# Performance work log

Hardware: AMD Instinct MI355X
Metric: run time of the kernel (lower is better)

The kernel has to match this reference:

```python
import jax, jax.numpy as jnp
import numpy as np

REF_MIC_IDX = 0
LOAD = 0.001 / np.sqrt(2.0)  # diagonal loading added to BOTH real and imag parts in the torch code


def setup_inputs() -> dict:
    key = jax.random.key(0)
    k1, k2, k3 = jax.random.split(key, 3)
    shape = (8, 2, 8, 600, 257)  # N, RI, C, T, F
    return {
        "mixture": jax.random.normal(k1, shape, dtype=jnp.float32),
        "target": jax.random.normal(k2, shape, dtype=jnp.float32),
        "noise": jax.random.normal(k3, shape, dtype=jnp.float32),
    }


def _to_complex(x):
    # (N, 2, C, T, F) RI-stacked -> (N, C, T, F) complex
    return jax.lax.complex(x[:, 0], x[:, 1])


def reference(mixture, target, noise):
    N, _, C, T, F = mixture.shape
    y = _to_complex(mixture)  # (N, C, T, F)
    v = _to_complex(noise)
    cdtype = y.dtype

    # Time-averaged spatial covariance: sum_t V V^H / T -> (N, F, C, C)
    # (fused; the original materializes per-frame C x C matrices then sums)
    phi_v = jnp.einsum("nctf,ndtf->nfcd", v, jnp.conj(v)) / T
    phi_y = jnp.einsum("nctf,ndtf->nfcd", y, jnp.conj(y)) / T

    eye = jnp.eye(C, dtype=cdtype)
    # torch adds LOAD*eye to both real and imag slices -> complex (1+1j)*LOAD*eye
    phi_v = phi_v + (LOAD * (1.0 + 1.0j)) * eye

    G = jnp.linalg.inv(phi_v) @ phi_y  # (N, F, C, C)

    # l = trace(G) - C, where torch subtracts scalar C from both RI parts
    l = jnp.trace(G, axis1=-2, axis2=-1) - (C * (1.0 + 1.0j))  # (N, F)

    # H = (1/l) * (G - I) e_ref  -> column ref_mic_idx of (G - I)
    Ge = (G - eye)[..., :, REF_MIC_IDX]  # (N, F, C)
    H = Ge / l[..., None]  # (N, F, C)

    # Beamform: X(n,t,f) = sum_c conj(H)_{n,f,c} * y_{n,c,t,f}
    X = jnp.einsum("nfc,nctf->ntf", jnp.conj(H), y)  # (N, T, F)

    # Output in RI-stacked form with singleton channel: (N, 2, 1, T, F)
    est = jnp.stack([jnp.real(X), jnp.imag(X)], axis=1)[:, :, None]
    return est
```

## Files before the change

### kernel.cpp

```cpp
#include <hip/hip_runtime.h>
#include <stdint.h>


constexpr int N_  = 8;
constexpr int C_  = 8;
constexpr int T_  = 600;
constexpr int F_  = 257;
constexpr int TF_  = T_ * F_;
constexpr int CTF_ = C_ * TF_;
constexpr int NSTR_ = 2 * CTF_;
constexpr int NF_  = N_ * F_;
constexpr int NPAIR_ = 36;
constexpr float LOADC_ = 7.0710678118654755e-4f;
constexpr float INV_T_ = 1.0f / 600.0f;

struct cx { float r, i; };
__device__ __forceinline__ cx cmul(cx a, cx b) { return {a.r*b.r - a.i*b.i, a.r*b.i + a.i*b.r}; }
__device__ __forceinline__ cx csub(cx a, cx b) { return {a.r - b.r, a.i - b.i}; }
__device__ __forceinline__ cx cconj(cx a) { return {a.r, -a.i}; }
__device__ __forceinline__ cx cinv(cx a) {
    float id = 1.0f / (a.r*a.r + a.i*a.i);
    return {a.r*id, -a.i*id};
}
__device__ __forceinline__ cx cmadd(cx acc, cx a, cx b) {
    acc.r += a.r*b.r - a.i*b.i;
    acc.i += a.r*b.i + a.i*b.r;
    return acc;
}

__device__ __forceinline__ void gload_lds4(const float* g, float* l) {
    __builtin_amdgcn_global_load_lds(
        (const __attribute__((address_space(1))) void*)g,
        (__attribute__((address_space(3))) void*)l,
        4, 0, 0);
}

#define VMWAIT(N) asm volatile("s_waitcnt vmcnt(" #N ")" ::: "memory")
#define LGKM0()   asm volatile("s_waitcnt lgkmcnt(0)" ::: "memory")

template<int TSPLIT>
__global__ __launch_bounds__(64, 1) void cov_partial(
        const float* __restrict__ mix, const float* __restrict__ noi,
        float* __restrict__ part) {
    constexpr int TCHUNK = T_ / TSPLIT;
    constexpr int P = 3;
    static_assert(TCHUNK % P == 0 && TCHUNK > P, "ring/chunk mismatch");

    __shared__ float S[P][16][64];

    const int lane = threadIdx.x;
    const int f = blockIdx.x * 64 + lane;
    if (f >= F_) return;
    const int n = blockIdx.y;
    const int z = blockIdx.z;
    const int m = z & 1;
    const int chunk = z >> 1;
    const float* src = (m ? mix : noi) + (size_t)n * NSTR_
                     + (size_t)(chunk * TCHUNK) * F_ + f;

    auto stage = [&](int s, int t) {
        const float* pg = src + (size_t)t * F_;
        float* lp = &S[s][0][0];
#pragma unroll
        for (int c = 0; c < C_; ++c) {
            gload_lds4(pg + (size_t)c * TF_,        lp + (2*c)   * 64);
            gload_lds4(pg + (size_t)c * TF_ + CTF_, lp + (2*c+1) * 64);
        }
    };

    float accr[NPAIR_], acci[NPAIR_];
#pragma unroll
    for (int p = 0; p < NPAIR_; ++p) { accr[p] = 0.f; acci[p] = 0.f; }

    auto consume = [&](int s) {
        float re[C_], im[C_];
#pragma unroll
        for (int c = 0; c < C_; ++c) {
            re[c] = S[s][2*c][lane];
            im[c] = S[s][2*c+1][lane];
        }
        int p = 0;
#pragma unroll
        for (int c = 0; c < C_; ++c) {
#pragma unroll
            for (int d = 0; d <= c; ++d, ++p) {
                accr[p] += re[c]*re[d] + im[c]*im[d];
                acci[p] += im[c]*re[d] - re[c]*im[d];
            }
        }
    };

    stage(0, 0); stage(1, 1); stage(2, 2);

    for (int tb = 0; tb < TCHUNK - P; tb += P) {
        VMWAIT(32); consume(0); LGKM0(); stage(0, tb + 3);
        VMWAIT(32); consume(1); LGKM0(); stage(1, tb + 4);
        VMWAIT(32); consume(2); LGKM0(); stage(2, tb + 5);
    }
    VMWAIT(32); consume(0);
    VMWAIT(16); consume(1);
    VMWAIT(0);  consume(2);

    float* out = part + (size_t)((m * TSPLIT + chunk) * 72) * NF_ + n * F_ + f;
#pragma unroll
    for (int p = 0; p < NPAIR_; ++p) {
        out[(size_t)(2*p)   * NF_] = accr[p];
        out[(size_t)(2*p+1) * NF_] = acci[p];
    }
}

__global__ __launch_bounds__(256) void reduce_cov(float* __restrict__ part, int tsplit) {
    int flat = blockIdx.x * 256 + threadIdx.x;
    constexpr int NQ4 = NF_ / 4;
    if (flat >= 2 * 72 * NQ4) return;
    int idx4 = flat % NQ4;
    int z = flat / NQ4;
    int m = z / 72;
    int q = z % 72;
    const float4* p4 = (const float4*)(part) + ((size_t)((m * tsplit) * 72 + q) * NF_) / 4 + idx4;
    float4 s = {0.f, 0.f, 0.f, 0.f};
    for (int ch = 0; ch < tsplit; ++ch) {
        float4 v = p4[(size_t)(ch * 72) * NF_ / 4];
        s.x += v.x; s.y += v.y; s.z += v.z; s.w += v.w;
    }
    *(float4*)((float*)part + (size_t)((m * tsplit) * 72 + q) * NF_ + idx4 * 4) = s;
}

__global__ __launch_bounds__(64, 1) void solve_w(
        const float* __restrict__ part, float* __restrict__ W, size_t yBase) {
    int idx = blockIdx.x * 64 + threadIdx.x;
    if (idx >= NF_) return;

    const float* pv = part + idx;
    const float* py = part + yBase + idx;

    cx M[64];
#pragma unroll
    for (int c = 0; c < 8; ++c) {
#pragma unroll
        for (int d = 0; d <= c; ++d) {
            int p = c*(c+1)/2 + d;
            cx val = { pv[(size_t)(2*p) * NF_] * INV_T_,
                       pv[(size_t)(2*p+1) * NF_] * INV_T_ };
            if (d == c) { val.r += LOADC_; val.i += LOADC_; }
            M[c*8 + d] = val;
            if (d < c) M[d*8 + c] = cconj(val);
        }
    }

#pragma unroll
    for (int k = 0; k < 8; ++k) {
        cx p = cinv(M[k*8 + k]);
        M[k*8 + k] = p;
#pragma unroll
        for (int j = 0; j < 8; ++j) {
            if (j != k) M[k*8 + j] = cmul(M[k*8 + j], p);
        }
#pragma unroll
        for (int i = 0; i < 8; ++i) {
            if (i == k) continue;
            cx fkt = M[i*8 + k];
#pragma unroll
            for (int j = 0; j < 8; ++j) {
                if (j != k) M[i*8 + j] = csub(M[i*8 + j], cmul(fkt, M[k*8 + j]));
            }
            cx t = cmul(fkt, p);
            M[i*8 + k] = { -t.r, -t.i };
        }
    }

    cx tr = {0.f, 0.f};
    cx g0[8];
#pragma unroll
    for (int c = 0; c < 8; ++c) g0[c] = (cx){0.f, 0.f};

#pragma unroll
    for (int a = 0; a < 8; ++a) {
#pragma unroll
        for (int b = 0; b <= a; ++b) {
            int p = a*(a+1)/2 + b;
            cx yv = { py[(size_t)(2*p) * NF_] * INV_T_,
                      py[(size_t)(2*p+1) * NF_] * INV_T_ };
            tr = cmadd(tr, M[b*8 + a], yv);
            if (a != b) tr = cmadd(tr, M[a*8 + b], cconj(yv));
            if (b == 0) {
#pragma unroll
                for (int i = 0; i < 8; ++i) g0[i] = cmadd(g0[i], M[i*8 + a], yv);
            }
        }
    }

    cx l = { tr.r - 8.0f, tr.i - 8.0f };
    float iden = 1.0f / (l.r*l.r + l.i*l.i);

    float* w = W + (size_t)idx * 16;
#pragma unroll
    for (int c = 0; c < 8; ++c) {
        cx ge = g0[c];
        if (c == 0) ge.r -= 1.0f;
        w[2*c]     = (ge.r*l.r + ge.i*l.i) * iden;
        w[2*c + 1] = (ge.r*l.i - ge.i*l.r) * iden;
    }
}

__global__ __launch_bounds__(256) void beamform(
        const float* __restrict__ mix, const float* __restrict__ W,
        float* __restrict__ out) {
    int n = blockIdx.y;
    int j = blockIdx.x * 256 + threadIdx.x;
    if (j >= TF_) return;
    int f = j % F_;

    const float4* w4 = (const float4*)(W + (size_t)(n * F_ + f) * 16);
    float4 q0 = w4[0], q1 = w4[1], q2 = w4[2], q3 = w4[3];
    float wv[16] = { q0.x, q0.y, q0.z, q0.w,
                     q1.x, q1.y, q1.z, q1.w,
                     q2.x, q2.y, q2.z, q2.w,
                     q3.x, q3.y, q3.z, q3.w };

    const float* base = mix + (size_t)n * NSTR_ + j;
    float xr = 0.f, xi = 0.f;
#pragma unroll
    for (int c = 0; c < C_; ++c) {
        float yr = base[(size_t)c * TF_];
        float yi = base[(size_t)c * TF_ + CTF_];
        float wr = wv[2*c], wi = wv[2*c + 1];
        xr += wr*yr - wi*yi;
        xi += wr*yi + wi*yr;
    }
    float* op = out + (size_t)n * (2 * TF_);
    op[j]       = xr;
    op[TF_ + j] = xi;
}

extern "C" void kernel_launch(void* const* d_in, const int* in_sizes, int n_in,
                              void* d_out, int out_size, void* d_ws, size_t ws_size,
                              hipStream_t stream) {
    const float* mix = (const float*)d_in[0];
    const float* noi = (const float*)d_in[2];

    const size_t need25 = ((size_t)2 * 25 * 72 * NF_ + (size_t)16 * NF_) * 4;
    float* part = (float*)d_ws;
    int tsplit;
    if (ws_size >= need25) {
        tsplit = 25;
        cov_partial<25><<<dim3(5, N_, 2 * 25), 64, 0, stream>>>(mix, noi, part);
    } else {
        tsplit = 20;
        cov_partial<20><<<dim3(5, N_, 2 * 20), 64, 0, stream>>>(mix, noi, part);
    }
    float* W = part + (size_t)2 * tsplit * 72 * NF_;

    reduce_cov<<<dim3((2 * 72 * (NF_ / 4) + 255) / 256), 256, 0, stream>>>(part, tsplit);
    solve_w<<<dim3((NF_ + 63) / 64), 64, 0, stream>>>(part, W, (size_t)tsplit * 72 * NF_);
    beamform<<<dim3((TF_ + 255) / 256, N_), 256, 0, stream>>>(mix, W, (float*)d_out);
}
```

Before: 282.3 us.

## Restructure covariance kernel into 256-thread blocks with register-staged double buffering

The covariance partial kernel moves from 64-thread blocks, each using async global-to-LDS loads through a 3-deep ring, to 256-thread blocks covering 128 or 129 frequencies. All threads load rows cooperatively into registers, write them to a double-buffered LDS tile and sync once per frame. This removes the nearly empty fifth frequency block per group and gives wider coalesced loads. In exchange, only about half of each block's threads do the accumulation, and it adds a block-wide barrier on every time step plus more register pressure from the launch bounds.

```diff
diff --git a/kernel.cpp b/kernel.cpp
--- a/kernel.cpp
+++ b/kernel.cpp
@@ -1,5 +1,4 @@
 #include <hip/hip_runtime.h>
-#include <stdint.h>
 
 
 constexpr int N_  = 8;
@@ -28,84 +27,101 @@
     return acc;
 }
 
-__device__ __forceinline__ void gload_lds4(const float* g, float* l) {
-    __builtin_amdgcn_global_load_lds(
-        (const __attribute__((address_space(1))) void*)g,
-        (__attribute__((address_space(3))) void*)l,
-        4, 0, 0);
-}
-
-#define VMWAIT(N) asm volatile("s_waitcnt vmcnt(" #N ")" ::: "memory")
-#define LGKM0()   asm volatile("s_waitcnt lgkmcnt(0)" ::: "memory")
-
 template<int TSPLIT>
-__global__ __launch_bounds__(64, 1) void cov_partial(
+__global__ __launch_bounds__(256, 3) void cov_partial(
         const float* __restrict__ mix, const float* __restrict__ noi,
         float* __restrict__ part) {
     constexpr int TCHUNK = T_ / TSPLIT;
-    constexpr int P = 3;
-    static_assert(TCHUNK % P == 0 && TCHUNK > P, "ring/chunk mismatch");
-
-    __shared__ float S[P][16][64];
-
-    const int lane = threadIdx.x;
-    const int f = blockIdx.x * 64 + lane;
-    if (f >= F_) return;
+
+    __shared__ float S[2][16][132];
+
+    const int tid = threadIdx.x;
+    const int hw  = tid >> 5;
+    const int l   = tid & 31;
+    const int fh    = blockIdx.x;
+    const int fbase = fh * 128;
+    const int FW    = fh ? (F_ - 128) : 128;
     const int n = blockIdx.y;
     const int z = blockIdx.z;
     const int m = z & 1;
     const int chunk = z >> 1;
+
     const float* src = (m ? mix : noi) + (size_t)n * NSTR_
-                     + (size_t)(chunk * TCHUNK) * F_ + f;
-
-    auto stage = [&](int s, int t) {
-        const float* pg = src + (size_t)t * F_;
-        float* lp = &S[s][0][0];
-#pragma unroll
-        for (int c = 0; c < C_; ++c) {
-            gload_lds4(pg + (size_t)c * TF_,        lp + (2*c)   * 64);
-            gload_lds4(pg + (size_t)c * TF_ + CTF_, lp + (2*c+1) * 64);
-        }
+                     + (size_t)(chunk * TCHUNK) * F_ + fbase;
+
+    size_t poff0, poff1;
+    {
+        const int r0 = hw, r1 = hw + 8;
+        poff0 = (size_t)(r0 >> 1) * TF_ + (size_t)(r0 & 1) * CTF_;
+        poff1 = (size_t)(r1 >> 1) * TF_ + (size_t)(r1 & 1) * CTF_;
+    }
+
+    float rg[2][4], tl[2];
+    auto stage = [&](int t) {
+        const float* row0 = src + poff0 + (size_t)t * F_;
+        const float* row1 = src + poff1 + (size_t)t * F_;
+#pragma unroll
+        for (int k = 0; k < 4; ++k) {
+            rg[0][k] = row0[l + 32*k];
+            rg[1][k] = row1[l + 32*k];
+        }
+        if (FW == 129 && l == 0) { tl[0] = row0[128]; tl[1] = row1[128]; }
     };
+    auto write_lds = [&](int buf) {
+        const int r0 = hw, r1 = hw + 8;
+#pragma unroll
+        for (int k = 0; k < 4; ++k) {
+            S[buf][r0][l + 32*k] = rg[0][k];
+            S[buf][r1][l + 32*k] = rg[1][k];
+        }
+        if (FW == 129 && l == 0) { S[buf][r0][128] = tl[0]; S[buf][r1][128] = tl[1]; }
+    };
 
     float accr[NPAIR_], acci[NPAIR_];
 #pragma unroll
     for (int p = 0; p < NPAIR_; ++p) { accr[p] = 0.f; acci[p] = 0.f; }
 
-    auto consume = [&](int s) {
-        float re[C_], im[C_];
-#pragma unroll
-        for (int c = 0; c < C_; ++c) {
-            re[c] = S[s][2*c][lane];
-            im[c] = S[s][2*c+1][lane];
-        }
-        int p = 0;
-#pragma unroll
-        for (int c = 0; c < C_; ++c) {
-#pragma unroll
-            for (int d = 0; d <= c; ++d, ++p) {
-                accr[p] += re[c]*re[d] + im[c]*im[d];
-                acci[p] += im[c]*re[d] - re[c]*im[d];
+    auto consume = [&](int buf) {
+        if (tid < FW) {
+            float re[C_], im[C_];
+#pragma unroll
+            for (int c = 0; c < C_; ++c) {
+                re[c] = S[buf][2*c][tid];
+                im[c] = S[buf][2*c+1][tid];
+            }
+            int p = 0;
+#pragma unroll
+            for (int c = 0; c < C_; ++c) {
+#pragma unroll
+                for (int d = 0; d <= c; ++d, ++p) {
+                    accr[p] += re[c]*re[d] + im[c]*im[d];
+                    acci[p] += im[c]*re[d] - re[c]*im[d];
+                }
             }
         }
     };
 
-    stage(0, 0); stage(1, 1); stage(2, 2);
-
-    for (int tb = 0; tb < TCHUNK - P; tb += P) {
-        VMWAIT(32); consume(0); LGKM0(); stage(0, tb + 3);
-        VMWAIT(32); consume(1); LGKM0(); stage(1, tb + 4);
-        VMWAIT(32); consume(2); LGKM0(); stage(2, tb + 5);
-    }
-    VMWAIT(32); consume(0);
-    VMWAIT(16); consume(1);
-    VMWAIT(0);  consume(2);
-
-    float* out = part + (size_t)((m * TSPLIT + chunk) * 72) * NF_ + n * F_ + f;
-#pragma unroll
-    for (int p = 0; p < NPAIR_; ++p) {
-        out[(size_t)(2*p)   * NF_] = accr[p];
-        out[(size_t)(2*p+1) * NF_] = acci[p];
+    stage(0);
+    write_lds(0);
+    __syncthreads();
+
+    for (int t = 0; t < TCHUNK; ++t) {
+        const int cur = t & 1;
+        const bool more = (t + 1 < TCHUNK);
+        if (more) stage(t + 1);
+        consume(cur);
+        if (more) write_lds(cur ^ 1);
+        __syncthreads();
+    }
+
+    if (tid < FW) {
+        const int f = fbase + tid;
+        float* out = part + (size_t)((m * TSPLIT + chunk) * 72) * NF_ + n * F_ + f;
+#pragma unroll
+        for (int p = 0; p < NPAIR_; ++p) {
+            out[(size_t)(2*p)   * NF_] = accr[p];
+            out[(size_t)(2*p+1) * NF_] = acci[p];
+        }
     }
 }
 
@@ -244,10 +260,10 @@
     int tsplit;
     if (ws_size >= need25) {
         tsplit = 25;
-        cov_partial<25><<<dim3(5, N_, 2 * 25), 64, 0, stream>>>(mix, noi, part);
+        cov_partial<25><<<dim3(2, N_, 2 * 25), 256, 0, stream>>>(mix, noi, part);
     } else {
         tsplit = 20;
-        cov_partial<20><<<dim3(5, N_, 2 * 20), 64, 0, stream>>>(mix, noi, part);
+        cov_partial<20><<<dim3(2, N_, 2 * 20), 256, 0, stream>>>(mix, noi, part);
     }
     float* W = part + (size_t)2 * tsplit * 72 * NF_;
 
```

After: 302.3 us. 1.07x slower.
